# Performance work log

Hardware: AMD Instinct MI355X
Metric: run time of the kernel (lower is better)

The kernel has to match this reference:

```python
import jax, jax.numpy as jnp
import numpy as np
from itertools import product as iter_product

N_QUBITS = 6
DIM = 2 ** N_QUBITS            # 64
N_GEN = DIM * DIM - 1          # 4095
DEPTH = 4
N_OBS = 15

_GENS = None

def _build_generators(n):
    I = np.eye(2, dtype=np.complex64)
    X = np.array([[0, 1], [1, 0]], np.complex64)
    Y = np.array([[0, -1j], [1j, 0]], np.complex64)
    Z = np.array([[1, 0], [0, -1]], np.complex64)
    P = [I, X, Y, Z]
    gens = []
    for idx in iter_product(range(4), repeat=n):
        if all(i == 0 for i in idx):
            continue
        m = P[idx[0]]
        for k in range(1, n):
            m = np.kron(m, P[idx[k]])
        gens.append(m)
    return jnp.asarray(np.stack(gens))  # [4^n-1, 2^n, 2^n] complex64

def _gens():
    global _GENS
    if _GENS is None:
        _GENS = _build_generators(N_QUBITS)
    return _GENS

def _apply_ry(psi, q, theta, n):
    # psi: [B, 2^n] complex; RY(theta) on qubit q
    B = psi.shape[0]
    x = psi.reshape(B, 2 ** q, 2, 2 ** (n - q - 1))
    c = jnp.cos(theta / 2)
    s = jnp.sin(theta / 2)
    s0, s1 = x[:, :, 0, :], x[:, :, 1, :]
    x = jnp.stack([c * s0 - s * s1, s * s0 + c * s1], axis=2)
    return x.reshape(B, -1)

def _apply_cnot(psi, c, t, n):
    # psi: [B, 2^n]; CNOT control c, target t
    B = psi.shape[0]
    x = psi.reshape((B,) + (2,) * n)
    ax_c, ax_t = 1 + c, 1 + t
    x0 = jnp.take(x, 0, axis=ax_c)
    x1 = jnp.take(x, 1, axis=ax_c)
    ax_t2 = ax_t - (1 if ax_t > ax_c else 0)
    x1 = jnp.flip(x1, axis=ax_t2)
    x = jnp.stack([x0, x1], axis=ax_c)
    return x.reshape(B, -1)

def _make_hermitians(A, B, D):
    # create_Hermitian vectorized over the m observables.
    # h[i,j] = A[idx]+iB[idx] for j<i (row-major lower-tri), h[i-1,i-1]=D[i];
    # then H = h + h^H.
    il, jl = jnp.tril_indices(DIM, -1)  # row-major order matches count+j loop
    di = jnp.arange(DIM - 1)

    def one(a, b, d):
        h = jnp.zeros((DIM, DIM), jnp.complex64)
        h = h.at[il, jl].set(a + 1j * b)
        h = h.at[di, di].set(d[1:].astype(jnp.complex64))
        return h + h.conj().T

    return jax.vmap(one)(A, B, D)  # [m, DIM, DIM]

def setup_inputs() -> dict:
    key = jax.random.key(0)
    ks = jax.random.split(key, 8)
    batch, input_dim, hidden = 256, 1024, 2047
    n_off = DIM * (DIM - 1) // 2  # 2016
    return {
        "x": jax.random.normal(ks[0], (batch, input_dim), jnp.float32),
        "W1": 0.02 * jax.random.normal(ks[1], (input_dim, hidden), jnp.float32),
        "b1": jnp.zeros((hidden,), jnp.float32),
        "W2": 0.02 * jax.random.normal(ks[2], (hidden, N_GEN), jnp.float32),
        "b2": jnp.zeros((N_GEN,), jnp.float32),
        "var_params": 0.01 * jax.random.normal(ks[3], (DEPTH, N_QUBITS), jnp.float32),
        "A": 2.0 * jax.random.normal(ks[4], (N_OBS, n_off), jnp.float32),
        "B": 2.0 * jax.random.normal(ks[5], (N_OBS, n_off), jnp.float32),
        "D": 2.0 * jax.random.normal(ks[6], (N_OBS, DIM), jnp.float32),
    }

def reference(x, W1, b1, W2, b2, var_params, A, B, D):
    n = N_QUBITS
    # encoding projection: Linear -> SiLU -> Linear
    h = jax.nn.silu(x @ W1 + b1)
    theta = h @ W2 + b2  # [batch, 4^n - 1]
    gens = _gens()  # [n_gen, dim, dim] complex64 (constant)
    # A_mat = sum_g theta_g G_g (Hermitian), U = exp(i A_mat)
    Amat = jnp.einsum('bg,gij->bij', theta.astype(jnp.complex64), gens)
    U = jax.vmap(jax.scipy.linalg.expm)(1j * Amat)  # [batch, dim, dim]
    psi = U[:, :, 0]  # apply to |0...0>
    # hardware-efficient VQC: RY layer + CNOT ring per depth
    for d in range(DEPTH):
        for q in range(n):
            psi = _apply_ry(psi, q, var_params[d, q], n)
        for q in range(n):
            psi = _apply_cnot(psi, q, (q + 1) % n, n)
    H = _make_hermitians(A, B, D)  # [m, dim, dim]
    # expectation <psi|H_w|psi>
    exp = jnp.einsum('bi,wij,bj->bw', psi.conj(), H, psi).real
    return exp  # [batch, n_observables]
```

## Files before the change

kernel.cpp:

```cpp
#include <hip/hip_runtime.h>
#include <math.h>

typedef unsigned short ushort_t;
typedef __attribute__((ext_vector_type(8))) short bf16x8_t;
typedef __attribute__((ext_vector_type(4))) float f32x4_t;

__device__ __forceinline__ void tsplit(float v, unsigned& h, unsigned& l) {
  unsigned u = __float_as_uint(v);
  h = u >> 16;
  float lo = v - __uint_as_float(u & 0xffff0000u);
  l = __float_as_uint(lo) >> 16;
}

__device__ __forceinline__ void transpose_tile(
    const float* __restrict__ W, ushort_t* __restrict__ Wh,
    ushort_t* __restrict__ Wl, int K, int N, int Kpad, int n0, int k0, int t) {
  __shared__ float sh[32][33];
  const int tx = t & 31, ty = t >> 5;
#pragma unroll
  for (int i = 0; i < 4; ++i) {
    int k = k0 + i * 8 + ty;
    float v = (k < K && (n0 + tx) < N) ? W[(size_t)k * N + n0 + tx] : 0.f;
    sh[tx][i * 8 + ty] = v;
  }
  __syncthreads();
  const int nn = t >> 3;
  const int kq = t & 7;
  unsigned h[4], l[4];
#pragma unroll
  for (int e = 0; e < 4; ++e) tsplit(sh[nn][kq * 4 + e], h[e], l[e]);
  size_t o = (size_t)(n0 + nn) * Kpad + k0 + kq * 4;
  uint2 ph, pl;
  ph.x = h[0] | (h[1] << 16); ph.y = h[2] | (h[3] << 16);
  pl.x = l[0] | (l[1] << 16); pl.y = l[2] | (l[3] << 16);
  *(uint2*)&Wh[o] = ph;
  *(uint2*)&Wl[o] = pl;
}

__global__ __launch_bounds__(256) void prep_kernel(
    const float* __restrict__ x, const float* __restrict__ W1,
    const float* __restrict__ W2,
    ushort_t* __restrict__ xh, ushort_t* __restrict__ xl,
    ushort_t* __restrict__ w1h, ushort_t* __restrict__ w1l,
    ushort_t* __restrict__ w2h, ushort_t* __restrict__ w2l) {
  const int bid = blockIdx.x;
  const int t = threadIdx.x;
  if (bid < 256) {
    int i4 = bid * 256 + t;
    float4 v = ((const float4*)x)[i4];
    unsigned h0, l0, h1, l1, h2, l2, h3, l3;
    tsplit(v.x, h0, l0); tsplit(v.y, h1, l1);
    tsplit(v.z, h2, l2); tsplit(v.w, h3, l3);
    uint2 ph, pl;
    ph.x = h0 | (h1 << 16); ph.y = h2 | (h3 << 16);
    pl.x = l0 | (l1 << 16); pl.y = l2 | (l3 << 16);
    ((uint2*)xh)[i4] = ph;
    ((uint2*)xl)[i4] = pl;
  } else if (bid < 256 + 2048) {
    int tau = bid - 256;
    transpose_tile(W1, w1h, w1l, 1024, 2047, 1024,
                   (tau & 63) * 32, (tau >> 6) * 32, t);
  } else {
    int tau = bid - 2304;
    transpose_tile(W2, w2h, w2l, 2047, 4095, 2048,
                   (tau & 127) * 32, (tau >> 7) * 32, t);
  }
}

#define LSTR 40
__global__ __launch_bounds__(256) void gemm_fused_kernel(
    const ushort_t* __restrict__ Ah, const ushort_t* __restrict__ Al,
    const ushort_t* __restrict__ Bh, const ushort_t* __restrict__ Bl,
    float* __restrict__ part, int KA, int KH, int Npad) {
  __shared__ ushort_t lds[4][64 * LSTR];
  const int t = threadIdx.x;
  const int lane = t & 63;
  const int wv = t >> 6;
  const int lane15 = lane & 15;
  const int quad = lane >> 4;
  const int wm = wv >> 1, wn = wv & 1;
  const int m0 = blockIdx.y * 64;
  const int n0 = blockIdx.x * 64;
  const int ks = blockIdx.z;

  const ushort_t* src = (wv == 0) ? Ah : (wv == 1) ? Al : (wv == 2) ? Bh : Bl;
  const int rowBase = (wv < 2) ? m0 : n0;
  ushort_t* dst = &lds[wv][0];

  f32x4_t acc[2][2];
#pragma unroll
  for (int i = 0; i < 2; ++i)
#pragma unroll
    for (int j = 0; j < 2; ++j) acc[i][j] = (f32x4_t){0.f, 0.f, 0.f, 0.f};

  const int iters = KH >> 5;
  const int kbase = ks * KH;
  for (int kt = 0; kt < iters; ++kt) {
    const int k0 = kbase + (kt << 5);
#pragma unroll
    for (int q = 0; q < 4; ++q) {
      int r = q * 16 + (lane >> 2);
      int c = (lane & 3) * 8;
      *(int4*)&dst[r * LSTR + c] =
          *(const int4*)(src + (size_t)(rowBase + r) * KA + k0 + c);
    }
    __syncthreads();
    bf16x8_t afh[2], afl[2], bfh[2], bfl[2];
#pragma unroll
    for (int i = 0; i < 2; ++i) {
      int mr = wm * 32 + i * 16 + lane15;
      afh[i] = *(const bf16x8_t*)&lds[0][mr * LSTR + quad * 8];
      afl[i] = *(const bf16x8_t*)&lds[1][mr * LSTR + quad * 8];
      int nr = wn * 32 + i * 16 + lane15;
      bfh[i] = *(const bf16x8_t*)&lds[2][nr * LSTR + quad * 8];
      bfl[i] = *(const bf16x8_t*)&lds[3][nr * LSTR + quad * 8];
    }
#pragma unroll
    for (int i = 0; i < 2; ++i)
#pragma unroll
      for (int j = 0; j < 2; ++j) {
        acc[i][j] = __builtin_amdgcn_mfma_f32_16x16x32_bf16(
            afh[i], bfh[j], acc[i][j], 0, 0, 0);
        acc[i][j] = __builtin_amdgcn_mfma_f32_16x16x32_bf16(
            afh[i], bfl[j], acc[i][j], 0, 0, 0);
        acc[i][j] = __builtin_amdgcn_mfma_f32_16x16x32_bf16(
            afl[i], bfh[j], acc[i][j], 0, 0, 0);
      }
    __syncthreads();
  }
  float* pbase = part + (size_t)ks * 256 * Npad;
#pragma unroll
  for (int i = 0; i < 2; ++i)
#pragma unroll
    for (int j = 0; j < 2; ++j) {
      int row0 = m0 + wm * 32 + i * 16 + quad * 4;
      int col = n0 + wn * 32 + j * 16 + lane15;
#pragma unroll
      for (int reg = 0; reg < 4; ++reg)
        pbase[(size_t)(row0 + reg) * Npad + col] = acc[i][j][reg];
    }
}

__global__ __launch_bounds__(256) void gemm2k_kernel(
    const ushort_t* __restrict__ Ah, const ushort_t* __restrict__ Al,
    const ushort_t* __restrict__ Bh, const ushort_t* __restrict__ Bl,
    float* __restrict__ part) {
  __shared__ ushort_t Ab[2][128 * LSTR];
  __shared__ ushort_t Bb[2][64 * LSTR];
  const int t = threadIdx.x;
  const int lane = t & 63;
  const int wv = t >> 6;
  const int l15 = lane & 15;
  const int quad = lane >> 4;
  const int wm = wv >> 1, wn = wv & 1;
  const int m0 = blockIdx.y * 128;
  const int n0 = blockIdx.x * 64;
  const int ks = blockIdx.z;

  f32x4_t acc[4][2];
#pragma unroll
  for (int i = 0; i < 4; ++i)
#pragma unroll
    for (int j = 0; j < 2; ++j) acc[i][j] = (f32x4_t){0.f, 0.f, 0.f, 0.f};

  for (int kt = 0; kt < 16; ++kt) {
    const int k0 = ks * 512 + kt * 32;
    if (wv < 2) {
      const ushort_t* src = wv ? Al : Ah;
      ushort_t* dst = Ab[wv];
#pragma unroll
      for (int q = 0; q < 8; ++q) {
        int r = q * 16 + (lane >> 2);
        int c = (lane & 3) * 8;
        *(int4*)&dst[r * LSTR + c] =
            *(const int4*)(src + (size_t)(m0 + r) * 2048 + k0 + c);
      }
    } else {
      const ushort_t* src = (wv == 3) ? Bl : Bh;
      ushort_t* dst = Bb[wv - 2];
#pragma unroll
      for (int q = 0; q < 4; ++q) {
        int r = q * 16 + (lane >> 2);
        int c = (lane & 3) * 8;
        *(int4*)&dst[r * LSTR + c] =
            *(const int4*)(src + (size_t)(n0 + r) * 2048 + k0 + c);
      }
    }
    __syncthreads();
    bf16x8_t bfh[2], bfl[2];
#pragma unroll
    for (int j = 0; j < 2; ++j) {
      int nr = wn * 32 + j * 16 + l15;
      bfh[j] = *(const bf16x8_t*)&Bb[0][nr * LSTR + quad * 8];
      bfl[j] = *(const bf16x8_t*)&Bb[1][nr * LSTR + quad * 8];
    }
#pragma unroll
    for (int i = 0; i < 4; ++i) {
      int mr = wm * 64 + i * 16 + l15;
      bf16x8_t afh = *(const bf16x8_t*)&Ab[0][mr * LSTR + quad * 8];
      bf16x8_t afl = *(const bf16x8_t*)&Ab[1][mr * LSTR + quad * 8];
#pragma unroll
      for (int j = 0; j < 2; ++j) {
        acc[i][j] = __builtin_amdgcn_mfma_f32_16x16x32_bf16(
            afh, bfh[j], acc[i][j], 0, 0, 0);
        acc[i][j] = __builtin_amdgcn_mfma_f32_16x16x32_bf16(
            afh, bfl[j], acc[i][j], 0, 0, 0);
        acc[i][j] = __builtin_amdgcn_mfma_f32_16x16x32_bf16(
            afl, bfh[j], acc[i][j], 0, 0, 0);
      }
    }
    __syncthreads();
  }
  float* pbase = part + (size_t)ks * 256 * 4096;
#pragma unroll
  for (int i = 0; i < 4; ++i)
#pragma unroll
    for (int j = 0; j < 2; ++j) {
      int row0 = m0 + wm * 64 + i * 16 + quad * 4;
      int col = n0 + wn * 32 + j * 16 + l15;
#pragma unroll
      for (int rg = 0; rg < 4; ++rg)
        pbase[(size_t)(row0 + rg) * 4096 + col] = acc[i][j][rg];
    }
}

__global__ __launch_bounds__(256) void reduce1_kernel(
    const float* __restrict__ p, const float* __restrict__ b1,
    ushort_t* __restrict__ hh, ushort_t* __restrict__ hl) {
  int idx = blockIdx.x * 256 + threadIdx.x;
  int n = idx & 2047;
  float v = p[idx] + p[idx + 256 * 2048];
  if (n < 2047) {
    v += b1[n];
    v = v / (1.f + expf(-v));
  } else {
    v = 0.f;
  }
  unsigned h, l;
  tsplit(v, h, l);
  hh[idx] = (ushort_t)h;
  hl[idx] = (ushort_t)l;
}

#define TM 64
#define TN 64
#define TK 16
__global__ __launch_bounds__(256) void gemm_tiled(
    const float* __restrict__ X, const float* __restrict__ W,
    const float* __restrict__ bias, float* __restrict__ out,
    int M, int N, int K, int ldx, int ldw, int ldo, int doSilu, int padN)
{
  __shared__ float Xs[TK][TM + 4];
  __shared__ float Ws[TK][TN + 4];
  const int t = threadIdx.x;
  const int n0 = blockIdx.x * TN;
  const int m0 = blockIdx.y * TM;
  const int tr = t >> 4, tc = t & 15;
  float acc[4][4];
#pragma unroll
  for (int i = 0; i < 4; ++i)
#pragma unroll
    for (int j = 0; j < 4; ++j) acc[i][j] = 0.f;
  const int xr = t >> 2, xk = (t & 3) * 4;
  const int wk = t >> 4, wc = (t & 15) * 4;
  for (int k0 = 0; k0 < K; k0 += TK) {
    {
      const float* xp = X + (size_t)(m0 + xr) * ldx + (k0 + xk);
      float xv[4];
      if (k0 + xk + 3 < K) {
        float4 v = *(const float4*)xp;
        xv[0] = v.x; xv[1] = v.y; xv[2] = v.z; xv[3] = v.w;
      } else {
#pragma unroll
        for (int e = 0; e < 4; ++e) xv[e] = (k0 + xk + e < K) ? xp[e] : 0.f;
      }
#pragma unroll
      for (int e = 0; e < 4; ++e) Xs[xk + e][xr] = xv[e];
    }
    {
      const int kk = k0 + wk;
      const float* wp = W + (size_t)kk * ldw + (n0 + wc);
      const bool kv = kk < K;
#pragma unroll
      for (int e = 0; e < 4; ++e) {
        int n = n0 + wc + e;
        Ws[wk][wc + e] = (kv && n < N) ? wp[e] : 0.f;
      }
    }
    __syncthreads();
#pragma unroll
    for (int k = 0; k < TK; ++k) {
      float4 av = *(const float4*)&Xs[k][tr * 4];
      float4 bv = *(const float4*)&Ws[k][tc * 4];
      float a4[4] = {av.x, av.y, av.z, av.w};
      float b4[4] = {bv.x, bv.y, bv.z, bv.w};
#pragma unroll
      for (int i = 0; i < 4; ++i)
#pragma unroll
        for (int j = 0; j < 4; ++j)
          acc[i][j] = fmaf(a4[i], b4[j], acc[i][j]);
    }
    __syncthreads();
  }
#pragma unroll
  for (int i = 0; i < 4; ++i) {
    const int mrow = m0 + tr * 4 + i;
    float* op = out + (size_t)mrow * ldo;
#pragma unroll
    for (int j = 0; j < 4; ++j) {
      const int n = n0 + tc * 4 + j;
      if (n < N) {
        float v = acc[i][j] + bias[n];
        if (doSilu) v = v / (1.f + expf(-v));
        op[n] = v;
      } else if (n < padN) {
        op[n] = 0.f;
      }
    }
  }
}

#define RS 72
#define PL (64 * RS)

__device__ __forceinline__ void qmm4(
    const ushort_t* __restrict__ Prm, const ushort_t* __restrict__ Qcm,
    float* ore, float* oim, int mt, int nt, int quad, int l15)
{
  f32x4_t aR = (f32x4_t){0.f, 0.f, 0.f, 0.f};
  f32x4_t aN = (f32x4_t){0.f, 0.f, 0.f, 0.f};
  f32x4_t aI = (f32x4_t){0.f, 0.f, 0.f, 0.f};
#pragma unroll
  for (int kb = 0; kb < 2; ++kb) {
    const int ko = kb * 32 + quad * 8;
    const int ra = (mt * 16 + l15) * RS + ko;
    bf16x8_t arh = *(const bf16x8_t*)&Prm[0 * PL + ra];
    bf16x8_t arl = *(const bf16x8_t*)&Prm[1 * PL + ra];
    bf16x8_t aih = *(const bf16x8_t*)&Prm[2 * PL + ra];
    bf16x8_t ail = *(const bf16x8_t*)&Prm[3 * PL + ra];
    const int rb = (nt * 16 + l15) * RS + ko;
    bf16x8_t brh = *(const bf16x8_t*)&Qcm[0 * PL + rb];
    bf16x8_t brl = *(const bf16x8_t*)&Qcm[1 * PL + rb];
    bf16x8_t bih = *(const bf16x8_t*)&Qcm[2 * PL + rb];
    bf16x8_t bil = *(const bf16x8_t*)&Qcm[3 * PL + rb];
    aR = __builtin_amdgcn_mfma_f32_16x16x32_bf16(arh, brh, aR, 0, 0, 0);
    aR = __builtin_amdgcn_mfma_f32_16x16x32_bf16(arh, brl, aR, 0, 0, 0);
    aR = __builtin_amdgcn_mfma_f32_16x16x32_bf16(arl, brh, aR, 0, 0, 0);
    aN = __builtin_amdgcn_mfma_f32_16x16x32_bf16(aih, bih, aN, 0, 0, 0);
    aN = __builtin_amdgcn_mfma_f32_16x16x32_bf16(aih, bil, aN, 0, 0, 0);
    aN = __builtin_amdgcn_mfma_f32_16x16x32_bf16(ail, bih, aN, 0, 0, 0);
    aI = __builtin_amdgcn_mfma_f32_16x16x32_bf16(arh, bih, aI, 0, 0, 0);
    aI = __builtin_amdgcn_mfma_f32_16x16x32_bf16(arh, bil, aI, 0, 0, 0);
    aI = __builtin_amdgcn_mfma_f32_16x16x32_bf16(arl, bih, aI, 0, 0, 0);
    aI = __builtin_amdgcn_mfma_f32_16x16x32_bf16(aih, brh, aI, 0, 0, 0);
    aI = __builtin_amdgcn_mfma_f32_16x16x32_bf16(aih, brl, aI, 0, 0, 0);
    aI = __builtin_amdgcn_mfma_f32_16x16x32_bf16(ail, brh, aI, 0, 0, 0);
  }
#pragma unroll
  for (int rg = 0; rg < 4; ++rg) {
    ore[rg] = aR[rg] - aN[rg];
    oim[rg] = aI[rg];
  }
}

__device__ __forceinline__ void stage_rm4(
    ushort_t* rm, const float* re, const float* im, int mt, int nt,
    int quad, int l15)
{
  unsigned rh[4], rl[4], ih[4], il[4];
#pragma unroll
  for (int rg = 0; rg < 4; ++rg) {
    tsplit(re[rg], rh[rg], rl[rg]);
    tsplit(im[rg], ih[rg], il[rg]);
  }
#pragma unroll
  for (int rg = 0; rg < 4; ++rg) {
    int idx = (mt * 16 + quad * 4 + rg) * RS + nt * 16 + l15;
    rm[0 * PL + idx] = (ushort_t)rh[rg];
    rm[1 * PL + idx] = (ushort_t)rl[rg];
    rm[2 * PL + idx] = (ushort_t)ih[rg];
    rm[3 * PL + idx] = (ushort_t)il[rg];
  }
}

__device__ __forceinline__ void stage_cm4(
    ushort_t* cm, const float* re, const float* im, int mt, int nt,
    int quad, int l15)
{
  unsigned rh[4], rl[4], ih[4], il[4];
#pragma unroll
  for (int rg = 0; rg < 4; ++rg) {
    tsplit(re[rg], rh[rg], rl[rg]);
    tsplit(im[rg], ih[rg], il[rg]);
  }
  int base = (nt * 16 + l15) * RS + mt * 16 + quad * 4;
  uint2 p;
  p.x = rh[0] | (rh[1] << 16); p.y = rh[2] | (rh[3] << 16);
  *(uint2*)&cm[0 * PL + base] = p;
  p.x = rl[0] | (rl[1] << 16); p.y = rl[2] | (rl[3] << 16);
  *(uint2*)&cm[1 * PL + base] = p;
  p.x = ih[0] | (ih[1] << 16); p.y = ih[2] | (ih[3] << 16);
  *(uint2*)&cm[2 * PL + base] = p;
  p.x = il[0] | (il[1] << 16); p.y = il[2] | (il[3] << 16);
  *(uint2*)&cm[3 * PL + base] = p;
}

__device__ __forceinline__ void stage_both4(
    ushort_t* rm, ushort_t* cm, const float* re, const float* im,
    int mt, int nt, int quad, int l15)
{
  stage_rm4(rm, re, im, mt, nt, quad, l15);
  stage_cm4(cm, re, im, mt, nt, quad, l15);
}

__global__ __launch_bounds__(1024, 4) void quantum_kernel(
    const float* __restrict__ pin,
    const float* __restrict__ b2g,
    const float* __restrict__ vp,
    const float* __restrict__ Aobs,
    const float* __restrict__ Bobs,
    const float* __restrict__ Dobs,
    float* __restrict__ out,
    int fused)
{
  __shared__ __align__(16) ushort_t PQ[2][8 * PL];
  __shared__ float ps[128];
  __shared__ float scr16[16];
  __shared__ float csb[24], snb[24];
  __shared__ float sAf;
  __shared__ int   sS;

  float*  thetas = (float*)&PQ[1][0];
  float2* Als    = (float2*)&PQ[0][0];

  const int t = threadIdx.x;
  const int b = blockIdx.x;
  const int lane = t & 63;
  const int w = t >> 6;
  const int quad = lane >> 4;
  const int l15 = lane & 15;
  const int mt = w >> 2, nt = w & 3;

  float ssq;
  {
    float4 v = ((const float4*)(pin + (size_t)b * 4096))[t];
    if (fused) {
#pragma unroll
      for (int k = 1; k < 4; ++k) {
        float4 u =
            ((const float4*)(pin + (size_t)k * 256 * 4096 + (size_t)b * 4096))[t];
        v.x += u.x; v.y += u.y; v.z += u.z; v.w += u.w;
      }
      int n0i = 4 * t;
      v.x += b2g[n0i];
      v.y += b2g[n0i + 1];
      v.z += b2g[n0i + 2];
      if (n0i + 3 < 4095) v.w += b2g[n0i + 3];
    }
    if (t == 1023) v.w = 0.f;
    thetas[4 * t + 0] = v.x; thetas[4 * t + 1] = v.y;
    thetas[4 * t + 2] = v.z; thetas[4 * t + 3] = v.w;
    ssq = v.x * v.x + v.y * v.y + v.z * v.z + v.w * v.w;
  }
#pragma unroll
  for (int mm = 1; mm < 64; mm <<= 1) ssq += __shfl_xor(ssq, mm);
  if (lane == 0) scr16[w] = ssq;
  __syncthreads();
  if (w == 0) {
    float s = (lane < 16) ? scr16[lane] : 0.f;
#pragma unroll
    for (int mm = 1; mm < 64; mm <<= 1) s += __shfl_xor(s, mm);
    if (lane == 0) {
      float frob = fmaxf(8.f * sqrtf(s), 1e-3f);
      sAf = frob;
      float bound = 0.30f * frob;
      int sc = (bound > 1.f) ? (int)ceilf(log2f(bound)) : 0;
      sS = sc < 0 ? 0 : (sc > 12 ? 12 : sc);
    }
  } else if (w == 1 && lane < 24) {
    float sn, cs;
    sincosf(vp[lane] * 0.5f, &sn, &cs);
    snb[lane] = sn;
    csb[lane] = cs;
  }
  __syncthreads();
  const int sPow = sS;

  for (int xx = 0; xx < 4; ++xx) {
    const int x = w + 16 * xx;
    const int z = lane;
    int g1 = 0;
#pragma unroll
    for (int bq = 0; bq < 6; ++bq) {
      int xb = (x >> bq) & 1, zb = (z >> bq) & 1;
      int dig = xb ? (zb ? 2 : 1) : (zb ? 3 : 0);
      g1 |= dig << (2 * bq);
    }
    float tv = (g1 == 0) ? 0.f : thetas[g1 - 1];
    int pc = __popc(x & z) & 3;
    float re, im;
    switch (pc) {
      case 0:  re = tv;  im = 0.f;  break;
      case 1:  re = 0.f; im = -tv;  break;
      case 2:  re = -tv; im = 0.f;  break;
      default: re = 0.f; im = tv;   break;
    }
#pragma unroll
    for (int mk = 1; mk < 64; mk <<= 1) {
      float ore = __shfl_xor(re, mk);
      float oim = __shfl_xor(im, mk);
      if (z & mk) { re = ore - re; im = oim - im; }
      else        { re = re + ore; im = im + oim; }
    }
    Als[z * 66 + (z ^ x)] = make_float2(re, im);
  }
  __syncthreads();

  const float scl = ldexpf(1.f, -sPow);
  float bre[4], bim[4];
#pragma unroll
  for (int rg = 0; rg < 4; ++rg) {
    int row = mt * 16 + quad * 4 + rg;
    int col = nt * 16 + l15;
    float2 v = Als[row * 66 + col];
    bre[rg] = -v.y * scl;
    bim[rg] =  v.x * scl;
  }
  __syncthreads();

  ushort_t* b0 = &PQ[0][0];
  ushort_t* b1 = &PQ[1][0];
  stage_both4(b0, b0 + 4 * PL, bre, bim, mt, nt, quad, l15);
  __syncthreads();
  float b2re[4], b2im[4];
  qmm4(b0, b0 + 4 * PL, b2re, b2im, mt, nt, quad, l15);
  stage_both4(b1, b1 + 4 * PL, b2re, b2im, mt, nt, quad, l15);
  __syncthreads();
  float b3re[4], b3im[4];
  qmm4(b1, b0 + 4 * PL, b3re, b3im, mt, nt, quad, l15);

  const float c3 = 1.f / 6.f, c4 = 1.f / 24.f, c5 = 1.f / 120.f;
  const float c6 = 1.f / 720.f, c7 = 1.f / 5040.f, c8 = 1.f / 40320.f;
  float s1re[4], s1im[4], p0re[4], p0im[4];
#pragma unroll
  for (int rg = 0; rg < 4; ++rg) {
    float dg = (mt == nt && l15 == quad * 4 + rg) ? 1.f : 0.f;
    s1re[rg] = c4 * dg + c5 * bre[rg] + c6 * b2re[rg] + c7 * b3re[rg];
    s1im[rg] =           c5 * bim[rg] + c6 * b2im[rg] + c7 * b3im[rg];
    p0re[rg] = dg + bre[rg] + 0.5f * b2re[rg] + c3 * b3re[rg];
    p0im[rg] =      bim[rg] + 0.5f * b2im[rg] + c3 * b3im[rg];
  }
  float b4re[4], b4im[4];
  qmm4(b1, b1 + 4 * PL, b4re, b4im, mt, nt, quad, l15);
#pragma unroll
  for (int rg = 0; rg < 4; ++rg) {
    s1re[rg] += c8 * b4re[rg];
    s1im[rg] += c8 * b4im[rg];
  }
  __syncthreads();
  stage_rm4(b0, s1re, s1im, mt, nt, quad, l15);
  stage_cm4(b0 + 4 * PL, b4re, b4im, mt, nt, quad, l15);
  __syncthreads();
  float ure[4], uim[4];
  qmm4(b0, b0 + 4 * PL, ure, uim, mt, nt, quad, l15);
#pragma unroll
  for (int rg = 0; rg < 4; ++rg) {
    ure[rg] += p0re[rg];
    uim[rg] += p0im[rg];
  }

  int cur = 1;
  for (int q = 0; q < sPow; ++q) {
    ushort_t* bb = &PQ[cur][0];
    stage_both4(bb, bb + 4 * PL, ure, uim, mt, nt, quad, l15);
    __syncthreads();
    qmm4(bb, bb + 4 * PL, ure, uim, mt, nt, quad, l15);
    cur ^= 1;
  }

  if (nt == 0 && l15 == 0) {
#pragma unroll
    for (int rg = 0; rg < 4; ++rg) {
      int row = mt * 16 + quad * 4 + rg;
      ps[2 * row] = ure[rg];
      ps[2 * row + 1] = uim[rg];
    }
  }
  __syncthreads();

  if (t < 64) {
    float pre = ps[2 * t], pim = ps[2 * t + 1];
#pragma unroll
    for (int d = 0; d < 4; ++d) {
#pragma unroll
      for (int q = 0; q < 6; ++q) {
        float s = snb[d * 6 + q], c = csb[d * 6 + q];
        int bpos = 5 - q;
        int bit = (t >> bpos) & 1;
        float ore = __shfl_xor(pre, 1 << bpos);
        float oim = __shfl_xor(pim, 1 << bpos);
        float sg = bit ? s : -s;
        pre = c * pre + sg * ore;
        pim = c * pim + sg * oim;
      }
#pragma unroll
      for (int q = 0; q < 6; ++q) {
        int bc = 5 - q;
        int bt = 5 - ((q + 1) % 6);
        float ore = __shfl_xor(pre, 1 << bt);
        float oim = __shfl_xor(pim, 1 << bt);
        int ctrl = (t >> bc) & 1;
        pre = ctrl ? ore : pre;
        pim = ctrl ? oim : pim;
      }
    }
    ps[2 * t] = pre; ps[2 * t + 1] = pim;
  }
  __syncthreads();

  float* Rt = (float*)&PQ[0][0];
  float* It = Rt + 2016;
  for (int p = t; p < 2016; p += 1024) {
    int i = (int)((1.f + sqrtf(8.f * (float)p + 1.f)) * 0.5f);
    while (i * (i - 1) / 2 > p) --i;
    while (i * (i + 1) / 2 <= p) ++i;
    int j = p - i * (i - 1) / 2;
    float pri = ps[2 * i], pii = ps[2 * i + 1];
    float prj = ps[2 * j], pij = ps[2 * j + 1];
    Rt[p] = pri * prj + pii * pij;
    It[p] = pri * pij - pii * prj;
  }
  __syncthreads();

  if (w < 15) {
    float xr = ps[2 * lane], xi = ps[2 * lane + 1];
    float mypsq = xr * xr + xi * xi;
    const float* Ap = Aobs + w * 2016;
    const float* Bp = Bobs + w * 2016;
    float part = 0.f;
    for (int p2 = lane; p2 < 1008; p2 += 64) {
      float2 a = *(const float2*)&Ap[2 * p2];
      float2 bb2 = *(const float2*)&Bp[2 * p2];
      float2 rt = *(const float2*)&Rt[2 * p2];
      float2 it = *(const float2*)&It[2 * p2];
      part += a.x * rt.x - bb2.x * it.x;
      part += a.y * rt.y - bb2.y * it.y;
    }
    if (lane < 63) part += Dobs[w * 64 + lane + 1] * mypsq;
#pragma unroll
    for (int mm = 1; mm < 64; mm <<= 1) part += __shfl_xor(part, mm);
    if (lane == 0) out[b * 15 + w] = 2.f * part;
  }
}

extern "C" void kernel_launch(void* const* d_in, const int* in_sizes, int n_in,
                              void* d_out, int out_size, void* d_ws, size_t ws_size,
                              hipStream_t stream) {
  const float* x  = (const float*)d_in[0];
  const float* W1 = (const float*)d_in[1];
  const float* b1 = (const float*)d_in[2];
  const float* W2 = (const float*)d_in[3];
  const float* b2 = (const float*)d_in[4];
  const float* vp = (const float*)d_in[5];
  const float* Ao = (const float*)d_in[6];
  const float* Bo = (const float*)d_in[7];
  const float* Do = (const float*)d_in[8];
  float* out = (float*)d_out;

  const size_t O_XH  = 0;
  const size_t O_XL  = 524288;
  const size_t O_W1H = 1048576;
  const size_t O_W1L = 5242880;
  const size_t O_PG1 = 9437184;
  const size_t O_PT  = 0;
  const size_t O_W2H = 16777216;
  const size_t O_W2L = 33554432;
  const size_t O_HH  = 50331648;
  const size_t O_HL  = 51380224;
  const size_t NEED  = 52428800;

  if (ws_size >= NEED) {
    char* ws = (char*)d_ws;
    ushort_t* xh  = (ushort_t*)(ws + O_XH);
    ushort_t* xl  = (ushort_t*)(ws + O_XL);
    ushort_t* w1h = (ushort_t*)(ws + O_W1H);
    ushort_t* w1l = (ushort_t*)(ws + O_W1L);
    float* partg1 = (float*)(ws + O_PG1);
    float* part16 = (float*)(ws + O_PT);
    ushort_t* w2h = (ushort_t*)(ws + O_W2H);
    ushort_t* w2l = (ushort_t*)(ws + O_W2L);
    ushort_t* hh  = (ushort_t*)(ws + O_HH);
    ushort_t* hl  = (ushort_t*)(ws + O_HL);

    prep_kernel<<<10496, 256, 0, stream>>>(x, W1, W2, xh, xl, w1h, w1l, w2h, w2l);
    gemm_fused_kernel<<<dim3(32, 4, 2), 256, 0, stream>>>(
        xh, xl, w1h, w1l, partg1, 1024, 512, 2048);
    reduce1_kernel<<<2048, 256, 0, stream>>>(partg1, b1, hh, hl);
    gemm2k_kernel<<<dim3(64, 2, 4), 256, 0, stream>>>(hh, hl, w2h, w2l, part16);
    quantum_kernel<<<256, 1024, 0, stream>>>(part16, b2, vp, Ao, Bo, Do, out, 1);
  } else {
    float* h     = (float*)d_ws;
    float* theta = h + 256 * 2048;
    gemm_tiled<<<dim3(32, 4), 256, 0, stream>>>(
        x, W1, b1, h, 256, 2047, 1024, 1024, 2047, 2048, 1, 2048);
    gemm_tiled<<<dim3(64, 4), 256, 0, stream>>>(
        h, W2, b2, theta, 256, 4095, 2047, 2048, 4095, 4096, 0, 4096);
    quantum_kernel<<<256, 1024, 0, stream>>>(theta, b2, vp, Ao, Bo, Do, out, 0);
  }
}
```

Measured before the change: 181.3 us.

## Fuse GEMM1 epilogue and co-schedule W2 transpose alongside GEMM1 blocks

The W2 transpose/split moves out of the prep kernel and into the GEMM1 launch, where extra blocks run it concurrently with the GEMM1 tiles. GEMM1 drops its split-K partial sums and uses smaller 32x64 tiles over the full K. Bias, SiLU and the hi/lo split now happen in its epilogue, which removes the reduce kernel and the partial-sum round trip through memory. In exchange each GEMM tile has a longer serial K loop with less reuse per block.

```diff
diff --git a/kernel.cpp b/kernel.cpp
--- a/kernel.cpp
+++ b/kernel.cpp
@@ -37,12 +37,10 @@
   *(uint2*)&Wl[o] = pl;
 }
 
-__global__ __launch_bounds__(256) void prep_kernel(
+__global__ __launch_bounds__(256) void prep2_kernel(
     const float* __restrict__ x, const float* __restrict__ W1,
-    const float* __restrict__ W2,
     ushort_t* __restrict__ xh, ushort_t* __restrict__ xl,
-    ushort_t* __restrict__ w1h, ushort_t* __restrict__ w1l,
-    ushort_t* __restrict__ w2h, ushort_t* __restrict__ w2l) {
+    ushort_t* __restrict__ w1h, ushort_t* __restrict__ w1l) {
   const int bid = blockIdx.x;
   const int t = threadIdx.x;
   if (bid < 256) {
@@ -56,89 +54,99 @@
     pl.x = l0 | (l1 << 16); pl.y = l2 | (l3 << 16);
     ((uint2*)xh)[i4] = ph;
     ((uint2*)xl)[i4] = pl;
-  } else if (bid < 256 + 2048) {
+  } else {
     int tau = bid - 256;
     transpose_tile(W1, w1h, w1l, 1024, 2047, 1024,
                    (tau & 63) * 32, (tau >> 6) * 32, t);
-  } else {
-    int tau = bid - 2304;
+  }
+}
+
+#define LSTR 40
+
+__global__ __launch_bounds__(256) void gemm1_w2t_kernel(
+    const ushort_t* __restrict__ xh, const ushort_t* __restrict__ xl,
+    const ushort_t* __restrict__ w1h, const ushort_t* __restrict__ w1l,
+    const float* __restrict__ b1,
+    ushort_t* __restrict__ hh, ushort_t* __restrict__ hl,
+    const float* __restrict__ W2,
+    ushort_t* __restrict__ w2h, ushort_t* __restrict__ w2l) {
+  const int bid = blockIdx.x;
+  const int t = threadIdx.x;
+  if (bid >= 256) {
+    int tau = bid - 256;
     transpose_tile(W2, w2h, w2l, 2047, 4095, 2048,
                    (tau & 127) * 32, (tau >> 7) * 32, t);
-  }
-}
-
-#define LSTR 40
-__global__ __launch_bounds__(256) void gemm_fused_kernel(
-    const ushort_t* __restrict__ Ah, const ushort_t* __restrict__ Al,
-    const ushort_t* __restrict__ Bh, const ushort_t* __restrict__ Bl,
-    float* __restrict__ part, int KA, int KH, int Npad) {
-  __shared__ ushort_t lds[4][64 * LSTR];
-  const int t = threadIdx.x;
+    return;
+  }
+  __shared__ ushort_t As[2][32 * LSTR];
+  __shared__ ushort_t Bs[2][64 * LSTR];
   const int lane = t & 63;
   const int wv = t >> 6;
-  const int lane15 = lane & 15;
+  const int l15 = lane & 15;
   const int quad = lane >> 4;
-  const int wm = wv >> 1, wn = wv & 1;
-  const int m0 = blockIdx.y * 64;
-  const int n0 = blockIdx.x * 64;
-  const int ks = blockIdx.z;
-
-  const ushort_t* src = (wv == 0) ? Ah : (wv == 1) ? Al : (wv == 2) ? Bh : Bl;
-  const int rowBase = (wv < 2) ? m0 : n0;
-  ushort_t* dst = &lds[wv][0];
-
-  f32x4_t acc[2][2];
-#pragma unroll
-  for (int i = 0; i < 2; ++i)
-#pragma unroll
-    for (int j = 0; j < 2; ++j) acc[i][j] = (f32x4_t){0.f, 0.f, 0.f, 0.f};
-
-  const int iters = KH >> 5;
-  const int kbase = ks * KH;
-  for (int kt = 0; kt < iters; ++kt) {
-    const int k0 = kbase + (kt << 5);
-#pragma unroll
-    for (int q = 0; q < 4; ++q) {
-      int r = q * 16 + (lane >> 2);
-      int c = (lane & 3) * 8;
-      *(int4*)&dst[r * LSTR + c] =
-          *(const int4*)(src + (size_t)(rowBase + r) * KA + k0 + c);
+  const int m0 = (bid >> 5) * 32;
+  const int n0 = (bid & 31) * 64;
+
+  f32x4_t acc[2];
+  acc[0] = (f32x4_t){0.f, 0.f, 0.f, 0.f};
+  acc[1] = (f32x4_t){0.f, 0.f, 0.f, 0.f};
+
+  for (int k0 = 0; k0 < 1024; k0 += 32) {
+    if (wv < 2) {
+      const ushort_t* src = wv ? xl : xh;
+      ushort_t* dst = As[wv];
+#pragma unroll
+      for (int q = 0; q < 2; ++q) {
+        int r = q * 16 + (lane >> 2);
+        int c = (lane & 3) * 8;
+        *(int4*)&dst[r * LSTR + c] =
+            *(const int4*)(src + (size_t)(m0 + r) * 1024 + k0 + c);
+      }
+    } else {
+      const ushort_t* src = (wv == 3) ? w1l : w1h;
+      ushort_t* dst = Bs[wv - 2];
+#pragma unroll
+      for (int q = 0; q < 4; ++q) {
+        int r = q * 16 + (lane >> 2);
+        int c = (lane & 3) * 8;
+        *(int4*)&dst[r * LSTR + c] =
+            *(const int4*)(src + (size_t)(n0 + r) * 1024 + k0 + c);
+      }
     }
     __syncthreads();
-    bf16x8_t afh[2], afl[2], bfh[2], bfl[2];
+    bf16x8_t bfh = *(const bf16x8_t*)&Bs[0][(wv * 16 + l15) * LSTR + quad * 8];
+    bf16x8_t bfl = *(const bf16x8_t*)&Bs[1][(wv * 16 + l15) * LSTR + quad * 8];
 #pragma unroll
     for (int i = 0; i < 2; ++i) {
-      int mr = wm * 32 + i * 16 + lane15;
-      afh[i] = *(const bf16x8_t*)&lds[0][mr * LSTR + quad * 8];
-      afl[i] = *(const bf16x8_t*)&lds[1][mr * LSTR + quad * 8];
-      int nr = wn * 32 + i * 16 + lane15;
-      bfh[i] = *(const bf16x8_t*)&lds[2][nr * LSTR + quad * 8];
-      bfl[i] = *(const bf16x8_t*)&lds[3][nr * LSTR + quad * 8];
-    }
-#pragma unroll
-    for (int i = 0; i < 2; ++i)
-#pragma unroll
-      for (int j = 0; j < 2; ++j) {
-        acc[i][j] = __builtin_amdgcn_mfma_f32_16x16x32_bf16(
-            afh[i], bfh[j], acc[i][j], 0, 0, 0);
-        acc[i][j] = __builtin_amdgcn_mfma_f32_16x16x32_bf16(
-            afh[i], bfl[j], acc[i][j], 0, 0, 0);
-        acc[i][j] = __builtin_amdgcn_mfma_f32_16x16x32_bf16(
-            afl[i], bfh[j], acc[i][j], 0, 0, 0);
-      }
+      int mr = i * 16 + l15;
+      bf16x8_t afh = *(const bf16x8_t*)&As[0][mr * LSTR + quad * 8];
+      bf16x8_t afl = *(const bf16x8_t*)&As[1][mr * LSTR + quad * 8];
+      acc[i] = __builtin_amdgcn_mfma_f32_16x16x32_bf16(afh, bfh, acc[i], 0, 0, 0);
+      acc[i] = __builtin_amdgcn_mfma_f32_16x16x32_bf16(afh, bfl, acc[i], 0, 0, 0);
+      acc[i] = __builtin_amdgcn_mfma_f32_16x16x32_bf16(afl, bfh, acc[i], 0, 0, 0);
+    }
     __syncthreads();
   }
-  float* pbase = part + (size_t)ks * 256 * Npad;
-#pragma unroll
-  for (int i = 0; i < 2; ++i)
-#pragma unroll
-    for (int j = 0; j < 2; ++j) {
-      int row0 = m0 + wm * 32 + i * 16 + quad * 4;
-      int col = n0 + wn * 32 + j * 16 + lane15;
-#pragma unroll
-      for (int reg = 0; reg < 4; ++reg)
-        pbase[(size_t)(row0 + reg) * Npad + col] = acc[i][j][reg];
-    }
+#pragma unroll
+  for (int i = 0; i < 2; ++i) {
+    int col = n0 + wv * 16 + l15;
+#pragma unroll
+    for (int rg = 0; rg < 4; ++rg) {
+      int row = m0 + i * 16 + quad * 4 + rg;
+      float v = acc[i][rg];
+      if (col < 2047) {
+        v += b1[col];
+        v = v / (1.f + expf(-v));
+      } else {
+        v = 0.f;
+      }
+      unsigned h, l;
+      tsplit(v, h, l);
+      size_t o = (size_t)row * 2048 + col;
+      hh[o] = (ushort_t)h;
+      hl[o] = (ushort_t)l;
+    }
+  }
 }
 
 __global__ __launch_bounds__(256) void gemm2k_kernel(
@@ -222,24 +230,6 @@
       for (int rg = 0; rg < 4; ++rg)
         pbase[(size_t)(row0 + rg) * 4096 + col] = acc[i][j][rg];
     }
-}
-
-__global__ __launch_bounds__(256) void reduce1_kernel(
-    const float* __restrict__ p, const float* __restrict__ b1,
-    ushort_t* __restrict__ hh, ushort_t* __restrict__ hl) {
-  int idx = blockIdx.x * 256 + threadIdx.x;
-  int n = idx & 2047;
-  float v = p[idx] + p[idx + 256 * 2048];
-  if (n < 2047) {
-    v += b1[n];
-    v = v / (1.f + expf(-v));
-  } else {
-    v = 0.f;
-  }
-  unsigned h, l;
-  tsplit(v, h, l);
-  hh[idx] = (ushort_t)h;
-  hl[idx] = (ushort_t)l;
 }
 
 #define TM 64
@@ -671,7 +661,6 @@
   const size_t O_XL  = 524288;
   const size_t O_W1H = 1048576;
   const size_t O_W1L = 5242880;
-  const size_t O_PG1 = 9437184;
   const size_t O_PT  = 0;
   const size_t O_W2H = 16777216;
   const size_t O_W2L = 33554432;
@@ -685,17 +674,15 @@
     ushort_t* xl  = (ushort_t*)(ws + O_XL);
     ushort_t* w1h = (ushort_t*)(ws + O_W1H);
     ushort_t* w1l = (ushort_t*)(ws + O_W1L);
-    float* partg1 = (float*)(ws + O_PG1);
     float* part16 = (float*)(ws + O_PT);
     ushort_t* w2h = (ushort_t*)(ws + O_W2H);
     ushort_t* w2l = (ushort_t*)(ws + O_W2L);
     ushort_t* hh  = (ushort_t*)(ws + O_HH);
     ushort_t* hl  = (ushort_t*)(ws + O_HL);
 
-    prep_kernel<<<10496, 256, 0, stream>>>(x, W1, W2, xh, xl, w1h, w1l, w2h, w2l);
-    gemm_fused_kernel<<<dim3(32, 4, 2), 256, 0, stream>>>(
-        xh, xl, w1h, w1l, partg1, 1024, 512, 2048);
-    reduce1_kernel<<<2048, 256, 0, stream>>>(partg1, b1, hh, hl);
+    prep2_kernel<<<2304, 256, 0, stream>>>(x, W1, xh, xl, w1h, w1l);
+    gemm1_w2t_kernel<<<8448, 256, 0, stream>>>(
+        xh, xl, w1h, w1l, b1, hh, hl, W2, w2h, w2l);
     gemm2k_kernel<<<dim3(64, 2, 4), 256, 0, stream>>>(hh, hl, w2h, w2l, part16);
     quantum_kernel<<<256, 1024, 0, stream>>>(part16, b2, vp, Ao, Bo, Do, out, 1);
   } else {
```

After: 174.7 us. 3.6% less time.
